# Performance work log

Measured on AMD Instinct MI355X. Metric: run time of the kernel, lower is better.

Reference implementation:

```python
import jax, jax.numpy as jnp
import numpy as np

WS = 16; HEADS = 6; TOPK = 64; KIN = 128; EPS = 1e-10
B, C, H, W = 1, 192, 192, 192
HID = 4 * C  # mlp_ratio * dim


def _ln(x, g, b):
    m = jnp.mean(x, axis=-1, keepdims=True)
    v = jnp.var(x, axis=-1, keepdims=True)
    return (x - m) * jax.lax.rsqrt(v + 1e-5) * g + b


def _dw_gelu(x, hw, w, b):
    # depthwise 5x5 conv + exact GELU on token sequence (B, N, C)
    Bx, N, Cx = x.shape
    h, wd = hw
    xi = x.transpose(0, 2, 1).reshape(Bx, Cx, h, wd)
    y = jax.lax.conv_general_dilated(xi, w, (1, 1), 'SAME',
        feature_group_count=Cx, dimension_numbers=('NCHW', 'OIHW', 'NCHW'))
    y = jax.nn.gelu(y + b[None, :, None, None], approximate=False)
    return y.reshape(Bx, Cx, N).transpose(0, 2, 1)


def _window_partition(x):
    b, h, w, c = x.shape
    x = x.reshape(b, h // WS, WS, w // WS, WS, c)
    return x.transpose(0, 1, 3, 2, 4, 5).reshape(-1, WS * WS, c)


def _window_reverse(win, h, w):
    c = win.shape[-1]
    b = win.shape[0] // ((h // WS) * (w // WS))
    x = win.reshape(b, h // WS, w // WS, WS, WS, c)
    return x.transpose(0, 1, 3, 2, 4, 5).reshape(b, h, w, c)


def setup_inputs():
    key = jax.random.key(0)
    ks = jax.random.split(key, 16)
    b_, n = B * (H // WS) * (W // WS), WS * WS
    wgen = lambda k, sh: jax.random.normal(k, sh, jnp.float32) * 0.02
    p = {}
    p['features_mv'] = jax.random.normal(ks[0], (B, C, H, W), jnp.float32)
    p['pfa_values'] = jax.random.uniform(ks[1], (b_, HEADS, n, KIN), jnp.float32)
    p['pfa_indices'] = jax.random.randint(ks[2], (b_, HEADS, n, KIN), 0, n, jnp.int32)
    p['rpi'] = jax.random.randint(ks[3], (n, n), 0, (2 * WS - 1) ** 2, jnp.int32)
    p['ln1_g'] = jnp.ones((C,)); p['ln1_b'] = jnp.zeros((C,))
    p['Wq_w'] = wgen(ks[4], (C, C)); p['Wq_b'] = jnp.zeros((C,))
    p['Wk_w'] = wgen(ks[5], (C, C)); p['Wk_b'] = jnp.zeros((C,))
    p['Wv_w'] = wgen(ks[6], (C, C)); p['Wv_b'] = jnp.zeros((C,))
    p['lepe_w'] = wgen(ks[7], (C, 1, 5, 5)); p['lepe_b'] = jnp.zeros((C,))
    p['rpb_table'] = wgen(ks[8], ((2 * WS - 1) ** 2, HEADS))
    p['proj_w'] = wgen(ks[9], (C, C)); p['proj_b'] = jnp.zeros((C,))
    p['ln2_g'] = jnp.ones((C,)); p['ln2_b'] = jnp.zeros((C,))
    p['fc1_w'] = wgen(ks[10], (C, HID)); p['fc1_b'] = jnp.zeros((HID,))
    p['ffn_dw_w'] = wgen(ks[11], (HID, 1, 5, 5)); p['ffn_dw_b'] = jnp.zeros((HID,))
    p['fc2_w'] = wgen(ks[12], (HID, C)); p['fc2_b'] = jnp.zeros((C,))
    return p


def reference(features_mv, pfa_values, pfa_indices, rpi, ln1_g, ln1_b,
              Wq_w, Wq_b, Wk_w, Wk_b, Wv_w, Wv_b, lepe_w, lepe_b, rpb_table,
              proj_w, proj_b, ln2_g, ln2_b, fc1_w, fc1_b, ffn_dw_w, ffn_dw_b,
              fc2_w, fc2_b):
    b, c, h, w = features_mv.shape
    hd = c // HEADS
    x = features_mv.reshape(b, c, h * w).transpose(0, 2, 1)  # (B, HW, C)
    shortcut = x
    xn = _ln(x, ln1_g, ln1_b)
    q = xn @ Wq_w + Wq_b
    k = xn @ Wk_w + Wk_b
    v = xn @ Wv_w + Wv_b
    vl = _dw_gelu(v, (h, w), lepe_w, lepe_b)  # v_LePE
    qkvp = jnp.concatenate([q, k, v, vl], axis=-1).reshape(b, h, w, 4 * c)
    xw = _window_partition(qkvp)  # (b_, n, 4C)
    b_, n = xw.shape[0], WS * WS
    qkvp = xw.reshape(b_, n, 4, HEADS, hd).transpose(2, 0, 3, 1, 4)
    q, k, v, vl = qkvp[0] * hd ** -0.5, qkvp[1], qkvp[2], qkvp[3]
    # SMM_QmK: per-query gathered q.k — dense scores then index gather
    scores = jnp.einsum('bhid,bhjd->bhij', q, k)          # (b_, H, n, n)
    attn = jnp.take_along_axis(scores, pfa_indices, axis=-1)  # (b_, H, n, K)
    # relative position bias, gathered by the same sparse indices
    rpb = rpb_table[rpi.reshape(-1)].reshape(n, n, HEADS).transpose(2, 0, 1)
    rpb_g = jnp.take_along_axis(jnp.broadcast_to(rpb[None], (b_, HEADS, n, n)),
                                pfa_indices, axis=-1)
    attn = jax.nn.softmax(attn + rpb_g, axis=-1)
    # progressive focused attention: multiply by prior values, renormalize
    attn = attn * pfa_values
    attn = (attn + EPS) / (jnp.sum(attn, axis=-1, keepdims=True) + EPS)
    # in-layer top-k reselection (topk=64 < KIN=128)
    tv, ti = jax.lax.top_k(attn, TOPK)
    idx = jnp.take_along_axis(pfa_indices, ti, axis=-1)   # (b_, H, n, TOPK)
    # SMM_AmV: scatter sparse attn to dense (duplicates sum) then matmul
    BH = b_ * HEADS
    a = tv.reshape(BH, n, TOPK)
    idxf = idx.reshape(BH, n, TOPK)
    dense = jnp.zeros((BH, n, n), tv.dtype).at[
        jnp.arange(BH)[:, None, None], jnp.arange(n)[None, :, None], idxf].add(a)
    xo = jnp.einsum('bij,bjd->bid', dense, v.reshape(BH, n, hd))
    xo = xo.reshape(b_, HEADS, n, hd) + vl
    xo = xo.transpose(0, 2, 1, 3).reshape(b_, n, c) @ proj_w + proj_b
    xr = _window_reverse(xo.reshape(-1, WS, WS, c), h, w)
    x = shortcut + xr.reshape(b, h * w, c)
    # ConvFFN
    y = _ln(x, ln2_g, ln2_b) @ fc1_w + fc1_b
    y = jax.nn.gelu(y, approximate=False)
    y = y + _dw_gelu(y, (h, w), ffn_dw_w, ffn_dw_b)
    x = x + (y @ fc2_w + fc2_b)
    return x
```

## Files before the change

kernel.cpp:

```cpp
#include <hip/hip_runtime.h>
#include <math.h>

#define HW 36864
#define CD 192
#define NH 6
#define HDIM 32
#define HIDD 768

typedef unsigned short u16;
typedef __attribute__((ext_vector_type(8))) short bf16x8;
typedef __attribute__((ext_vector_type(4))) float f32x4;

__device__ __forceinline__ float gelu_f(float x) {
  return 0.5f * x * (1.0f + erff(x * 0.70710678118654752f));
}
__device__ __forceinline__ u16 f2b(float f) {
  union { float f; unsigned u; } v; v.f = f;
  unsigned r = v.u + 0x7fff + ((v.u >> 16) & 1);
  return (u16)(r >> 16);
}
__device__ __forceinline__ float b2f(u16 b) {
  union { unsigned u; float f; } v; v.u = ((unsigned)b) << 16;
  return v.f;
}
__device__ __forceinline__ unsigned pack_hi16(unsigned w_lo, unsigned w_hi) {
  return __builtin_amdgcn_perm(w_hi, w_lo, 0x07060302u);
}

__global__ __launch_bounds__(256)
void lnt_kernel(const float* __restrict__ in, const float* __restrict__ g,
                const float* __restrict__ b, u16* __restrict__ outTM)
{
  __shared__ float tile[64][193];
  __shared__ float red[64][8];
  __shared__ float2 stat2[64];
  __shared__ float gb[384];
  const int tid = threadIdx.x;
  const int part = tid >> 6, tk = tid & 63;
  const int tok = blockIdx.x * 64 + tk;
  if (tid < 192) { gb[tid] = g[tid]; gb[192 + tid] = b[tid]; }
  float s = 0.f, sq = 0.f;
  for (int c = part * 48; c < part * 48 + 48; ++c) {
    float v = in[(size_t)c * HW + tok];
    tile[tk][c] = v; s += v; sq += v * v;
  }
  red[tk][part] = s; red[tk][4 + part] = sq;
  __syncthreads();
  if (tid < 64) {
    float ss = red[tid][0] + red[tid][1] + red[tid][2] + red[tid][3];
    float qq = red[tid][4] + red[tid][5] + red[tid][6] + red[tid][7];
    float m = ss * (1.0f / CD);
    float var = fmaxf(qq * (1.0f / CD) - m * m, 0.f);
    stat2[tid] = make_float2(m, rsqrtf(var + 1e-5f));
  }
  __syncthreads();
  unsigned* op = (unsigned*)outTM + (size_t)blockIdx.x * 6144;
  #pragma unroll
  for (int r = 0; r < 24; ++r) {
    int idx = tid + r * 256;
    int tok2 = idx / 96, dc = idx - tok2 * 96;
    float2 st = stat2[tok2];
    int c = dc * 2;
    float v0 = (tile[tok2][c] - st.x) * st.y * gb[c] + gb[192 + c];
    float v1 = (tile[tok2][c + 1] - st.x) * st.y * gb[c + 1] + gb[192 + c + 1];
    op[idx] = (unsigned)f2b(v0) | ((unsigned)f2b(v1) << 16);
  }
}

__global__ __launch_bounds__(256)
void trans_kernel(const u16* __restrict__ in, u16* __restrict__ out, int C)
{
  __shared__ u16 ls[64][34];
  const int m0 = blockIdx.x * 64, c0 = blockIdx.y * 32;
  const int t = threadIdx.x;
  #pragma unroll
  for (int r = 0; r < 4; ++r) {
    int idx = t + r * 256;
    int c = idx >> 5, dm = idx & 31;
    unsigned d = *(const unsigned*)(in + (size_t)(c0 + c) * HW + m0 + dm * 2);
    ls[dm * 2][c] = (u16)d;
    ls[dm * 2 + 1][c] = (u16)(d >> 16);
  }
  __syncthreads();
  #pragma unroll
  for (int r = 0; r < 4; ++r) {
    int idx = t + r * 256;
    int m = idx >> 4, dc = idx & 15;
    unsigned d = (unsigned)ls[m][dc * 2] | ((unsigned)ls[m][dc * 2 + 1] << 16);
    *(unsigned*)(out + (size_t)(m0 + m) * C + c0 + dc * 2) = d;
  }
}

__global__ __launch_bounds__(256)
void wtrans_kernel(const float* __restrict__ in, u16* __restrict__ out, int K, int N)
{
  __shared__ float ls[32][33];
  const int k0 = blockIdx.x * 32, n0 = blockIdx.y * 32;
  const int t = threadIdx.x;
  #pragma unroll
  for (int r = 0; r < 4; ++r) {
    int idx = t + r * 256;
    int k = idx >> 5, n = idx & 31;
    ls[k][n] = in[(size_t)(k0 + k) * N + n0 + n];
  }
  __syncthreads();
  #pragma unroll
  for (int r = 0; r < 4; ++r) {
    int idx = t + r * 256;
    int n = idx >> 5, k = idx & 31;
    out[(size_t)(n0 + n) * K + k0 + k] = f2b(ls[k][n]);
  }
}

__global__ __launch_bounds__(256)
void wtrans4_kernel(const float* __restrict__ w0, const float* __restrict__ w1,
                    const float* __restrict__ w2, const float* __restrict__ w3,
                    u16* __restrict__ out)
{
  __shared__ float ls[32][33];
  const int z = blockIdx.z;
  const float* in = (z == 0) ? w0 : (z == 1 ? w1 : (z == 2 ? w2 : w3));
  u16* op = out + (size_t)z * CD * CD;
  const int k0 = blockIdx.x * 32, n0 = blockIdx.y * 32;
  const int t = threadIdx.x;
  #pragma unroll
  for (int r = 0; r < 4; ++r) {
    int idx = t + r * 256;
    int k = idx >> 5, n = idx & 31;
    ls[k][n] = in[(size_t)(k0 + k) * CD + n0 + n];
  }
  __syncthreads();
  #pragma unroll
  for (int r = 0; r < 4; ++r) {
    int idx = t + r * 256;
    int n = idx >> 5, k = idx & 31;
    op[(size_t)(n0 + n) * CD + k0 + k] = f2b(ls[k][n]);
  }
}

template<int MODE>
__global__ __launch_bounds__(256, 4)
void mgemm_kernel(const u16* __restrict__ A,
                  const u16* __restrict__ W0, const u16* __restrict__ W1, const u16* __restrict__ W2,
                  const float* __restrict__ b0, const float* __restrict__ b1, const float* __restrict__ b2,
                  const float* __restrict__ aux, void* __restrict__ outv,
                  int K, int segN)
{
  const int n0 = blockIdx.x * 64;
  const int m0 = blockIdx.y * 128;
  const int seg = n0 / segN;
  const u16* Wp = (seg == 0) ? W0 : (seg == 1 ? W1 : W2);
  const float* biasp = (seg == 0) ? b0 : (seg == 1 ? b1 : b2);
  const int nl0 = n0 - seg * segN;

  __shared__ u16 As[128 * 32];
  __shared__ u16 Bs[64 * 32];

  const int tid = threadIdx.x;
  const int lane = tid & 63, wave = tid >> 6;
  const int wm = (wave >> 1) * 64, wn = (wave & 1) * 32;
  const int fm = lane & 15, fq = lane >> 4;
  const int ar = tid >> 2, akq = tid & 3;

  f32x4 acc[4][2];
  #pragma unroll
  for (int i = 0; i < 4; ++i) { acc[i][0] = (f32x4)(0.f); acc[i][1] = (f32x4)(0.f); }

  uint4 rA0, rA1, rB, nA0, nA1, nB;
  rA0 = *(const uint4*)(A + (size_t)(m0 + ar) * K + akq * 8);
  rA1 = *(const uint4*)(A + (size_t)(m0 + ar + 64) * K + akq * 8);
  rB  = *(const uint4*)(Wp + (size_t)(nl0 + ar) * K + akq * 8);

  for (int k0 = 0; k0 < K; k0 += 32) {
    *(uint4*)(&As[ar * 32 + akq * 8]) = rA0;
    *(uint4*)(&As[(ar + 64) * 32 + akq * 8]) = rA1;
    *(uint4*)(&Bs[ar * 32 + akq * 8]) = rB;
    __syncthreads();
    const int kn = (k0 + 32 < K) ? k0 + 32 : k0;
    nA0 = *(const uint4*)(A + (size_t)(m0 + ar) * K + kn + akq * 8);
    nA1 = *(const uint4*)(A + (size_t)(m0 + ar + 64) * K + kn + akq * 8);
    nB  = *(const uint4*)(Wp + (size_t)(nl0 + ar) * K + kn + akq * 8);
    bf16x8 af[4], bf[2];
    #pragma unroll
    for (int mt = 0; mt < 4; ++mt)
      af[mt] = *(const bf16x8*)(&As[(wm + mt * 16 + fm) * 32 + fq * 8]);
    #pragma unroll
    for (int nt = 0; nt < 2; ++nt)
      bf[nt] = *(const bf16x8*)(&Bs[(wn + nt * 16 + fm) * 32 + fq * 8]);
    #pragma unroll
    for (int mt = 0; mt < 4; ++mt)
      #pragma unroll
      for (int nt = 0; nt < 2; ++nt)
        acc[mt][nt] = __builtin_amdgcn_mfma_f32_16x16x32_bf16(af[mt], bf[nt], acc[mt][nt], 0, 0, 0);
    __syncthreads();
    rA0 = nA0; rA1 = nA1; rB = nB;
  }

  #pragma unroll
  for (int nt = 0; nt < 2; ++nt) {
    const int n = n0 + wn + nt * 16 + fm;
    const float bia = biasp[nl0 + wn + nt * 16 + fm];
    #pragma unroll
    for (int mt = 0; mt < 4; ++mt) {
      const int mb = m0 + wm + mt * 16 + fq * 4;
      float o[4];
      #pragma unroll
      for (int r = 0; r < 4; ++r) o[r] = acc[mt][nt][r] + bia;
      if (MODE == 0) {
        const float sc = (seg == 0) ? 0.17677669529663689f : 1.0f;
        u16 h0 = f2b(o[0] * sc), h1 = f2b(o[1] * sc), h2 = f2b(o[2] * sc), h3 = f2b(o[3] * sc);
        uint2 pk = make_uint2((unsigned)h0 | ((unsigned)h1 << 16), (unsigned)h2 | ((unsigned)h3 << 16));
        *(uint2*)((u16*)outv + (size_t)n * HW + mb) = pk;
      } else if (MODE == 1) {
        const float4 ax = *(const float4*)(aux + (size_t)n * HW + mb);
        *(float4*)((float*)outv + (size_t)n * HW + mb) =
            make_float4(o[0] + ax.x, o[1] + ax.y, o[2] + ax.z, o[3] + ax.w);
      } else if (MODE == 2) {
        u16 h0 = f2b(gelu_f(o[0])), h1 = f2b(gelu_f(o[1]));
        u16 h2 = f2b(gelu_f(o[2])), h3 = f2b(gelu_f(o[3]));
        uint2 pk = make_uint2((unsigned)h0 | ((unsigned)h1 << 16), (unsigned)h2 | ((unsigned)h3 << 16));
        *(uint2*)((u16*)outv + (size_t)n * HW + mb) = pk;
      } else {
        const float4 ax = *(const float4*)(aux + (size_t)n * HW + mb);
        float* op = (float*)outv;
        op[(size_t)(mb + 0) * CD + n] = o[0] + ax.x;
        op[(size_t)(mb + 1) * CD + n] = o[1] + ax.y;
        op[(size_t)(mb + 2) * CD + n] = o[2] + ax.z;
        op[(size_t)(mb + 3) * CD + n] = o[3] + ax.w;
      }
    }
  }
}

template<bool ADD>
__global__ __launch_bounds__(256)
void dwconv_kernel(const u16* __restrict__ in, const float* __restrict__ w,
                   const float* __restrict__ bias, u16* __restrict__ out)
{
  const int plane = blockIdx.z;
  const int bx = blockIdx.x * 64, by = blockIdx.y * 4;
  __shared__ float tile[8][68];
  __shared__ float ws[26];
  const int tid = threadIdx.x;
  if (tid < 26) ws[tid] = (tid < 25) ? w[plane * 25 + tid] : bias[plane];
  const u16* ip = in + (size_t)plane * HW;
  for (int e = tid; e < 544; e += 256) {
    int r = e / 68, cc = e - r * 68;
    int gy = by + r - 2, gx = bx + cc - 2;
    tile[r][cc] = (gy >= 0 && gy < 192 && gx >= 0 && gx < 192) ? b2f(ip[gy * 192 + gx]) : 0.f;
  }
  __syncthreads();
  const int tx = tid & 63, ty = tid >> 6;
  float acc = 0.f;
  #pragma unroll
  for (int dy = 0; dy < 5; ++dy)
    #pragma unroll
    for (int dx = 0; dx < 5; ++dx)
      acc = fmaf(tile[ty + dy][tx + dx], ws[dy * 5 + dx], acc);
  float v = gelu_f(acc + ws[25]);
  if (ADD) v += tile[ty + 2][tx + 2];
  out[(size_t)plane * HW + (by + ty) * 192 + bx + tx] = f2b(v);
}

__global__ __launch_bounds__(512, 6)
void attn_kernel(const u16* __restrict__ qg, const u16* __restrict__ kg,
                 const u16* __restrict__ vg, const u16* __restrict__ vlg,
                 const float* __restrict__ pfa_v, const int* __restrict__ pfa_i,
                 const int* __restrict__ rpi, const float* __restrict__ rpb_t,
                 u16* __restrict__ attn_out)
{
  const int h = blockIdx.x;
  const int win = blockIdx.y;
  const int wy = (win / 12) * 16;
  const int wx = (win - (win / 12) * 12) * 16;
  const size_t hb = (size_t)h * HDIM * HW;

  __shared__ u16 vT[32][264];
  __shared__ float Sb[32][262];
  __shared__ float rpb_h[964];

  const int tid = threadIdx.x;
  const int lane = tid & 63, wave = tid >> 6;
  const int fm = lane & 15, fq = lane >> 4;

  for (int r = tid; r < 961; r += 512) rpb_h[r] = rpb_t[r * 6 + h];

  u16* kst = (u16*)&Sb[0][0];
  #pragma unroll
  for (int r = 0; r < 8; ++r) {
    int idx = tid + r * 512;
    int d = idx >> 7, jp = idx & 127, j = jp * 2;
    int pg = (wy + (j >> 4)) * 192 + (wx + (j & 15));
    ushort2 kv = *(const ushort2*)(kg + hb + (size_t)d * HW + pg);
    kst[j * 32 + d] = kv.x; kst[(j + 1) * 32 + d] = kv.y;
    *(ushort2*)&vT[d][j] = *(const ushort2*)(vg + hb + (size_t)d * HW + pg);
  }
  __syncthreads();

  bf16x8 kf[4];
  #pragma unroll
  for (int t = 0; t < 4; ++t) {
    const int j0 = ((wave >> 1) * 4 + t) * 16;
    kf[t] = *(const bf16x8*)&kst[(j0 + fm) * 32 + fq * 8];
  }

  const size_t wb = ((size_t)win * NH + h) * 256;
  const unsigned long long lmlt = (1ull << lane) - 1ull;

  for (int pass = 0; pass < 8; ++pass) {
    union { bf16x8 v; u16 hh[8]; } aqu;
    {
      const int pgq = (wy + pass * 2 + (wave & 1)) * 192 + wx + fm;
      #pragma unroll
      for (int e = 0; e < 8; ++e)
        aqu.hh[e] = qg[hb + (size_t)(fq * 8 + e) * HW + pgq];
    }
    __syncthreads();

    int pj1[4], pj2[4]; float pv1[4], pv2[4];
    #pragma unroll
    for (int u = 0; u < 4; ++u) {
      const int i = pass * 32 + u * 8 + wave;
      const size_t base = (wb + (size_t)i) * 128;
      pj1[u] = pfa_i[base + lane];  pj2[u] = pfa_i[base + 64 + lane];
      pv1[u] = pfa_v[base + lane];  pv2[u] = pfa_v[base + 64 + lane];
    }

    #pragma unroll
    for (int t = 0; t < 4; ++t) {
      f32x4 c = __builtin_amdgcn_mfma_f32_16x16x32_bf16(aqu.v, kf[t], (f32x4)(0.f), 0, 0, 0);
      const int col = ((wave >> 1) * 4 + t) * 16 + fm;
      const int rowb = (wave & 1) * 16 + fq * 4;
      Sb[rowb + 0][col] = c[0]; Sb[rowb + 1][col] = c[1];
      Sb[rowb + 2][col] = c[2]; Sb[rowb + 3][col] = c[3];
    }
    __syncthreads();

    float rb1[4], rb2[4];
    #pragma unroll
    for (int u = 0; u < 4; ++u) {
      const int i = pass * 32 + u * 8 + wave;
      rb1[u] = rpb_h[rpi[i * 256 + pj1[u]]];
      rb2[u] = rpb_h[rpi[i * 256 + pj2[u]]];
    }
    float s1[4], s2[4];
    #pragma unroll
    for (int u = 0; u < 4; ++u) {
      const int iq = u * 8 + wave;
      s1[u] = Sb[iq][pj1[u]] + rb1[u];
      s2[u] = Sb[iq][pj2[u]] + rb2[u];
    }
    {
      const float2 z2 = make_float2(0.f, 0.f);
      #pragma unroll
      for (int u = 0; u < 4; ++u) {
        const int iq = u * 8 + wave;
        *(float2*)&Sb[iq][lane * 4]     = z2;
        *(float2*)&Sb[iq][lane * 4 + 2] = z2;
      }
    }
    float mx[4];
    #pragma unroll
    for (int u = 0; u < 4; ++u) mx[u] = fmaxf(s1[u], s2[u]);
    #pragma unroll
    for (int o = 32; o > 0; o >>= 1)
      #pragma unroll
      for (int u = 0; u < 4; ++u) mx[u] = fmaxf(mx[u], __shfl_xor(mx[u], o));
    float e1[4], e2[4], sA[4], sB[4];
    #pragma unroll
    for (int u = 0; u < 4; ++u) {
      e1[u] = expf(s1[u] - mx[u]); e2[u] = expf(s2[u] - mx[u]);
      sA[u] = e1[u] + e2[u];
      sB[u] = e1[u] * pv1[u] + e2[u] * pv2[u];
    }
    #pragma unroll
    for (int o = 32; o > 0; o >>= 1)
      #pragma unroll
      for (int u = 0; u < 4; ++u) { sA[u] += __shfl_xor(sA[u], o); sB[u] += __shfl_xor(sB[u], o); }
    unsigned ub1[4], ub2[4]; float a1[4], a2[4];
    #pragma unroll
    for (int u = 0; u < 4; ++u) {
      const float rs = 1.0f / sA[u];
      const float rden = 1.0f / (sB[u] * rs + 1e-10f);
      a1[u] = (e1[u] * rs * pv1[u] + 1e-10f) * rden;
      a2[u] = (e2[u] * rs * pv2[u] + 1e-10f) * rden;
      ub1[u] = __float_as_uint(a1[u]); ub2[u] = __float_as_uint(a2[u]);
    }
    unsigned thr[4] = {0u, 0u, 0u, 0u};
    #pragma unroll 1
    for (int bit = 30; bit >= 0; --bit) {
      #pragma unroll
      for (int u = 0; u < 4; ++u) {
        const unsigned cand = thr[u] | (1u << bit);
        const int cnt = (int)__popcll(__ballot(ub1[u] >= cand)) +
                        (int)__popcll(__ballot(ub2[u] >= cand));
        thr[u] = (cnt >= 64) ? cand : thr[u];
      }
    }
    #pragma unroll
    for (int u = 0; u < 4; ++u) {
      const int iq = u * 8 + wave;
      const bool gt1 = ub1[u] > thr[u], gt2 = ub2[u] > thr[u];
      const bool eq1 = ub1[u] == thr[u], eq2 = ub2[u] == thr[u];
      const unsigned long long meq1 = __ballot(eq1), meq2 = __ballot(eq2);
      const int need = 64 - (int)__popcll(__ballot(gt1)) - (int)__popcll(__ballot(gt2));
      const bool sel1 = gt1 || (eq1 && (int)__popcll(meq1 & lmlt) < need);
      const bool sel2 = gt2 || (eq2 && ((int)__popcll(meq1) + (int)__popcll(meq2 & lmlt)) < need);
      if (sel1) atomicAdd(&Sb[iq][pj1[u]], a1[u]);
      if (sel2) atomicAdd(&Sb[iq][pj2[u]], a2[u]);
    }
    __syncthreads();

    if (wave < 4) {
      const int mt = wave & 1, nt = wave >> 1;
      f32x4 acc = (f32x4)(0.f);
      #pragma unroll
      for (int k0 = 0; k0 < 8; ++k0) {
        const bf16x8 av = *(const bf16x8*)&vT[mt * 16 + fm][k0 * 32 + fq * 8];
        const float* pr = &Sb[nt * 16 + fm][k0 * 32 + fq * 8];
        const float2 p01 = *(const float2*)(pr + 0);
        const float2 p23 = *(const float2*)(pr + 2);
        const float2 p45 = *(const float2*)(pr + 4);
        const float2 p67 = *(const float2*)(pr + 6);
        const unsigned u0 = __float_as_uint(p01.x), u1 = __float_as_uint(p01.y);
        const unsigned u2 = __float_as_uint(p23.x), u3 = __float_as_uint(p23.y);
        const unsigned u4 = __float_as_uint(p45.x), u5 = __float_as_uint(p45.y);
        const unsigned u6 = __float_as_uint(p67.x), u7 = __float_as_uint(p67.y);
        union { bf16x8 v; unsigned q[4]; } bh, bl;
        bh.q[0] = pack_hi16(u0, u1); bh.q[1] = pack_hi16(u2, u3);
        bh.q[2] = pack_hi16(u4, u5); bh.q[3] = pack_hi16(u6, u7);
        const float l0 = p01.x - __uint_as_float(u0 & 0xffff0000u);
        const float l1 = p01.y - __uint_as_float(u1 & 0xffff0000u);
        const float l2 = p23.x - __uint_as_float(u2 & 0xffff0000u);
        const float l3 = p23.y - __uint_as_float(u3 & 0xffff0000u);
        const float l4 = p45.x - __uint_as_float(u4 & 0xffff0000u);
        const float l5 = p45.y - __uint_as_float(u5 & 0xffff0000u);
        const float l6 = p67.x - __uint_as_float(u6 & 0xffff0000u);
        const float l7 = p67.y - __uint_as_float(u7 & 0xffff0000u);
        bl.q[0] = pack_hi16(__float_as_uint(l0), __float_as_uint(l1));
        bl.q[1] = pack_hi16(__float_as_uint(l2), __float_as_uint(l3));
        bl.q[2] = pack_hi16(__float_as_uint(l4), __float_as_uint(l5));
        bl.q[3] = pack_hi16(__float_as_uint(l6), __float_as_uint(l7));
        acc = __builtin_amdgcn_mfma_f32_16x16x32_bf16(av, bh.v, acc, 0, 0, 0);
        acc = __builtin_amdgcn_mfma_f32_16x16x32_bf16(av, bl.v, acc, 0, 0, 0);
      }
      const int pg = (wy + pass * 2 + nt) * 192 + wx + fm;
      const int d0 = mt * 16 + fq * 4;
      const float r0 = acc[0] + b2f(vlg[hb + (size_t)(d0 + 0) * HW + pg]);
      const float r1 = acc[1] + b2f(vlg[hb + (size_t)(d0 + 1) * HW + pg]);
      const float r2 = acc[2] + b2f(vlg[hb + (size_t)(d0 + 2) * HW + pg]);
      const float r3 = acc[3] + b2f(vlg[hb + (size_t)(d0 + 3) * HW + pg]);
      const unsigned o01 = (unsigned)f2b(r0) | ((unsigned)f2b(r1) << 16);
      const unsigned o23 = (unsigned)f2b(r2) | ((unsigned)f2b(r3) << 16);
      *(uint2*)(attn_out + (size_t)pg * CD + h * HDIM + d0) = make_uint2(o01, o23);
    }
  }
}

extern "C" void kernel_launch(void* const* d_in, const int* in_sizes, int n_in,
                              void* d_out, int out_size, void* d_ws, size_t ws_size,
                              hipStream_t stream)
{
  (void)in_sizes; (void)n_in; (void)out_size; (void)ws_size;
  const float* features = (const float*)d_in[0];
  const float* pfa_v    = (const float*)d_in[1];
  const int*   pfa_i    = (const int*)d_in[2];
  const int*   rpi      = (const int*)d_in[3];
  const float* ln1_g    = (const float*)d_in[4];
  const float* ln1_b    = (const float*)d_in[5];
  const float* Wq_w     = (const float*)d_in[6];
  const float* Wq_b     = (const float*)d_in[7];
  const float* Wk_w     = (const float*)d_in[8];
  const float* Wk_b     = (const float*)d_in[9];
  const float* Wv_w     = (const float*)d_in[10];
  const float* Wv_b     = (const float*)d_in[11];
  const float* lepe_w   = (const float*)d_in[12];
  const float* lepe_b   = (const float*)d_in[13];
  const float* rpb_t    = (const float*)d_in[14];
  const float* proj_w   = (const float*)d_in[15];
  const float* proj_b   = (const float*)d_in[16];
  const float* ln2_g    = (const float*)d_in[17];
  const float* ln2_b    = (const float*)d_in[18];
  const float* fc1_w    = (const float*)d_in[19];
  const float* fc1_b    = (const float*)d_in[20];
  const float* dw_w     = (const float*)d_in[21];
  const float* dw_b     = (const float*)d_in[22];
  const float* fc2_w    = (const float*)d_in[23];
  const float* fc2_b    = (const float*)d_in[24];

  char* ws = (char*)d_ws;
  const size_t S  = (size_t)HW * CD;
  const size_t SB = S * 4;
  u16*   xnt    = (u16*)(ws);
  u16*   qkvb   = (u16*)(ws + SB / 2);
  u16*   q_ = qkvb; u16* k_ = qkvb + S; u16* v_ = qkvb + 2 * S;
  u16*   vl     = (u16*)(ws + 2 * SB);
  u16*   attn_o = (u16*)(ws + 2 * SB + SB / 2);
  float* x2     = (float*)(ws + 3 * SB);
  u16*   xn2t   = (u16*)(ws + 4 * SB);
  u16*   y_     = (u16*)(ws + 4 * SB + SB / 2);
  u16*   y2_    = (u16*)(ws + 6 * SB + SB / 2);
  u16*   y2t    = (u16*)(ws);
  u16*   wqt  = (u16*)(ws + 8 * SB + SB / 2);
  u16*   wkt  = wqt + 36864;
  u16*   wvt  = wkt + 36864;
  u16*   wpt  = wvt + 36864;
  u16*   wf1t = wpt + 36864;
  u16*   wf2t = wf1t + 147456;
  float* out = (float*)d_out;

  wtrans4_kernel<<<dim3(6, 6, 4), 256, 0, stream>>>(Wq_w, Wk_w, Wv_w, proj_w, wqt);
  wtrans_kernel<<<dim3(6, 24), 256, 0, stream>>>(fc1_w, wf1t, 192, 768);
  wtrans_kernel<<<dim3(24, 6), 256, 0, stream>>>(fc2_w, wf2t, 768, 192);
  lnt_kernel<<<dim3(HW / 64), 256, 0, stream>>>(features, ln1_g, ln1_b, xnt);
  mgemm_kernel<0><<<dim3(9, HW / 128), 256, 0, stream>>>(xnt, wqt, wkt, wvt, Wq_b, Wk_b, Wv_b,
                                                         nullptr, qkvb, 192, 192);
  dwconv_kernel<false><<<dim3(3, 48, 192), 256, 0, stream>>>(v_, lepe_w, lepe_b, vl);
  attn_kernel<<<dim3(6, 144), 512, 0, stream>>>(q_, k_, v_, vl, pfa_v, pfa_i, rpi, rpb_t, attn_o);
  mgemm_kernel<1><<<dim3(3, HW / 128), 256, 0, stream>>>(attn_o, wpt, wpt, wpt, proj_b, proj_b, proj_b,
                                                         features, x2, 192, 1 << 30);
  lnt_kernel<<<dim3(HW / 64), 256, 0, stream>>>(x2, ln2_g, ln2_b, xn2t);
  mgemm_kernel<2><<<dim3(12, HW / 128), 256, 0, stream>>>(xn2t, wf1t, wf1t, wf1t, fc1_b, fc1_b, fc1_b,
                                                          nullptr, y_, 192, 1 << 30);
  dwconv_kernel<true><<<dim3(3, 48, 768), 256, 0, stream>>>(y_, dw_w, dw_b, y2_);
  trans_kernel<<<dim3(HW / 64, 24), 256, 0, stream>>>(y2_, y2t, HIDD);
  mgemm_kernel<3><<<dim3(3, HW / 128), 256, 0, stream>>>(y2t, wf2t, wf2t, wf2t, fc2_b, fc2_b, fc2_b,
                                                         x2, out, 768, 1 << 30);
}
```

Baseline: 835.3 us.

## Prefetch attention inputs, shorten top-k radix search, use single fp16 MFMA for AV

```diff
diff --git a/kernel.cpp b/kernel.cpp
--- a/kernel.cpp
+++ b/kernel.cpp
@@ -10,6 +10,8 @@
 typedef unsigned short u16;
 typedef __attribute__((ext_vector_type(8))) short bf16x8;
 typedef __attribute__((ext_vector_type(4))) float f32x4;
+typedef __attribute__((ext_vector_type(8))) _Float16 f16x8;
+typedef __attribute__((ext_vector_type(2))) __fp16 fp16x2;
 
 __device__ __forceinline__ float gelu_f(float x) {
   return 0.5f * x * (1.0f + erff(x * 0.70710678118654752f));
@@ -23,8 +25,10 @@
   union { unsigned u; float f; } v; v.u = ((unsigned)b) << 16;
   return v.f;
 }
-__device__ __forceinline__ unsigned pack_hi16(unsigned w_lo, unsigned w_hi) {
-  return __builtin_amdgcn_perm(w_hi, w_lo, 0x07060302u);
+__device__ __forceinline__ unsigned pkrtz_u(float a, float b) {
+  union { fp16x2 h; unsigned u; } cv;
+  cv.h = __builtin_amdgcn_cvt_pkrtz(a, b);
+  return cv.u;
 }
 
 __global__ __launch_bounds__(256)
@@ -275,15 +279,15 @@
   const int wx = (win - (win / 12) * 12) * 16;
   const size_t hb = (size_t)h * HDIM * HW;
 
+  __shared__ float Sb[32][262];
   __shared__ u16 vT[32][264];
-  __shared__ float Sb[32][262];
-  __shared__ float rpb_h[964];
+  __shared__ u16 rpb_h[962];
 
   const int tid = threadIdx.x;
   const int lane = tid & 63, wave = tid >> 6;
   const int fm = lane & 15, fq = lane >> 4;
 
-  for (int r = tid; r < 961; r += 512) rpb_h[r] = rpb_t[r * 6 + h];
+  for (int r = tid; r < 961; r += 512) rpb_h[r] = f2b(rpb_t[r * 6 + h]);
 
   u16* kst = (u16*)&Sb[0][0];
   #pragma unroll
@@ -292,8 +296,9 @@
     int d = idx >> 7, jp = idx & 127, j = jp * 2;
     int pg = (wy + (j >> 4)) * 192 + (wx + (j & 15));
     ushort2 kv = *(const ushort2*)(kg + hb + (size_t)d * HW + pg);
-    kst[j * 32 + d] = kv.x; kst[(j + 1) * 32 + d] = kv.y;
-    *(ushort2*)&vT[d][j] = *(const ushort2*)(vg + hb + (size_t)d * HW + pg);
+    kst[j * 40 + d] = kv.x; kst[(j + 1) * 40 + d] = kv.y;
+    ushort2 vv = *(const ushort2*)(vg + hb + (size_t)d * HW + pg);
+    *(unsigned*)&vT[d][j] = pkrtz_u(b2f(vv.x), b2f(vv.y));
   }
   __syncthreads();
 
@@ -301,11 +306,20 @@
   #pragma unroll
   for (int t = 0; t < 4; ++t) {
     const int j0 = ((wave >> 1) * 4 + t) * 16;
-    kf[t] = *(const bf16x8*)&kst[(j0 + fm) * 32 + fq * 8];
+    kf[t] = *(const bf16x8*)&kst[(j0 + fm) * 40 + fq * 8];
   }
 
   const size_t wb = ((size_t)win * NH + h) * 256;
   const unsigned long long lmlt = (1ull << lane) - 1ull;
+  const unsigned KMASK = 0xFFFFF800u;
+
+  int pj1[4], pj2[4]; float pv1[4], pv2[4];
+  #pragma unroll
+  for (int u = 0; u < 4; ++u) {
+    const size_t base = (wb + (size_t)(u * 8 + wave)) * 128;
+    pj1[u] = pfa_i[base + lane];  pj2[u] = pfa_i[base + 64 + lane];
+    pv1[u] = pfa_v[base + lane];  pv2[u] = pfa_v[base + 64 + lane];
+  }
 
   for (int pass = 0; pass < 8; ++pass) {
     union { bf16x8 v; u16 hh[8]; } aqu;
@@ -315,15 +329,23 @@
       for (int e = 0; e < 8; ++e)
         aqu.hh[e] = qg[hb + (size_t)(fq * 8 + e) * HW + pgq];
     }
+    float vlv[4];
+    if (wave < 4) {
+      const int mt = wave & 1, nt = wave >> 1;
+      const int pgo = (wy + pass * 2 + nt) * 192 + wx + fm;
+      const int d0 = mt * 16 + fq * 4;
+      #pragma unroll
+      for (int e = 0; e < 4; ++e)
+        vlv[e] = b2f(vlg[hb + (size_t)(d0 + e) * HW + pgo]);
+    }
     __syncthreads();
 
-    int pj1[4], pj2[4]; float pv1[4], pv2[4];
+    int rbi1[4], rbi2[4];
     #pragma unroll
     for (int u = 0; u < 4; ++u) {
       const int i = pass * 32 + u * 8 + wave;
-      const size_t base = (wb + (size_t)i) * 128;
-      pj1[u] = pfa_i[base + lane];  pj2[u] = pfa_i[base + 64 + lane];
-      pv1[u] = pfa_v[base + lane];  pv2[u] = pfa_v[base + 64 + lane];
+      rbi1[u] = rpi[i * 256 + pj1[u]];
+      rbi2[u] = rpi[i * 256 + pj2[u]];
     }
 
     #pragma unroll
@@ -336,19 +358,12 @@
     }
     __syncthreads();
 
-    float rb1[4], rb2[4];
-    #pragma unroll
-    for (int u = 0; u < 4; ++u) {
-      const int i = pass * 32 + u * 8 + wave;
-      rb1[u] = rpb_h[rpi[i * 256 + pj1[u]]];
-      rb2[u] = rpb_h[rpi[i * 256 + pj2[u]]];
-    }
     float s1[4], s2[4];
     #pragma unroll
     for (int u = 0; u < 4; ++u) {
       const int iq = u * 8 + wave;
-      s1[u] = Sb[iq][pj1[u]] + rb1[u];
-      s2[u] = Sb[iq][pj2[u]] + rb2[u];
+      s1[u] = Sb[iq][pj1[u]] + b2f(rpb_h[rbi1[u]]);
+      s2[u] = Sb[iq][pj2[u]] + b2f(rpb_h[rbi2[u]]);
     }
     {
       const float2 z2 = make_float2(0.f, 0.f);
@@ -388,7 +403,7 @@
     }
     unsigned thr[4] = {0u, 0u, 0u, 0u};
     #pragma unroll 1
-    for (int bit = 30; bit >= 0; --bit) {
+    for (int bit = 29; bit >= 11; --bit) {
       #pragma unroll
       for (int u = 0; u < 4; ++u) {
         const unsigned cand = thr[u] | (1u << bit);
@@ -400,8 +415,9 @@
     #pragma unroll
     for (int u = 0; u < 4; ++u) {
       const int iq = u * 8 + wave;
-      const bool gt1 = ub1[u] > thr[u], gt2 = ub2[u] > thr[u];
-      const bool eq1 = ub1[u] == thr[u], eq2 = ub2[u] == thr[u];
+      const unsigned kb1 = ub1[u] & KMASK, kb2 = ub2[u] & KMASK;
+      const bool gt1 = kb1 > thr[u], gt2 = kb2 > thr[u];
+      const bool eq1 = kb1 == thr[u], eq2 = kb2 == thr[u];
       const unsigned long long meq1 = __ballot(eq1), meq2 = __ballot(eq2);
       const int need = 64 - (int)__popcll(__ballot(gt1)) - (int)__popcll(__ballot(gt2));
       const bool sel1 = gt1 || (eq1 && (int)__popcll(meq1 & lmlt) < need);
@@ -409,6 +425,16 @@
       if (sel1) atomicAdd(&Sb[iq][pj1[u]], a1[u]);
       if (sel2) atomicAdd(&Sb[iq][pj2[u]], a2[u]);
     }
+    int npj1[4], npj2[4]; float npv1[4], npv2[4];
+    {
+      const int pnext = (pass + 1) & 7;
+      #pragma unroll
+      for (int u = 0; u < 4; ++u) {
+        const size_t base = (wb + (size_t)(pnext * 32 + u * 8 + wave)) * 128;
+        npj1[u] = pfa_i[base + lane];  npj2[u] = pfa_i[base + 64 + lane];
+        npv1[u] = pfa_v[base + lane];  npv2[u] = pfa_v[base + 64 + lane];
+      }
+    }
     __syncthreads();
 
     if (wave < 4) {
@@ -416,43 +442,33 @@
       f32x4 acc = (f32x4)(0.f);
       #pragma unroll
       for (int k0 = 0; k0 < 8; ++k0) {
-        const bf16x8 av = *(const bf16x8*)&vT[mt * 16 + fm][k0 * 32 + fq * 8];
+        const f16x8 av = *(const f16x8*)&vT[mt * 16 + fm][k0 * 32 + fq * 8];
         const float* pr = &Sb[nt * 16 + fm][k0 * 32 + fq * 8];
         const float2 p01 = *(const float2*)(pr + 0);
         const float2 p23 = *(const float2*)(pr + 2);
         const float2 p45 = *(const float2*)(pr + 4);
         const float2 p67 = *(const float2*)(pr + 6);
-        const unsigned u0 = __float_as_uint(p01.x), u1 = __float_as_uint(p01.y);
-        const unsigned u2 = __float_as_uint(p23.x), u3 = __float_as_uint(p23.y);
-        const unsigned u4 = __float_as_uint(p45.x), u5 = __float_as_uint(p45.y);
-        const unsigned u6 = __float_as_uint(p67.x), u7 = __float_as_uint(p67.y);
-        union { bf16x8 v; unsigned q[4]; } bh, bl;
-        bh.q[0] = pack_hi16(u0, u1); bh.q[1] = pack_hi16(u2, u3);
-        bh.q[2] = pack_hi16(u4, u5); bh.q[3] = pack_hi16(u6, u7);
-        const float l0 = p01.x - __uint_as_float(u0 & 0xffff0000u);
-        const float l1 = p01.y - __uint_as_float(u1 & 0xffff0000u);
-        const float l2 = p23.x - __uint_as_float(u2 & 0xffff0000u);
-        const float l3 = p23.y - __uint_as_float(u3 & 0xffff0000u);
-        const float l4 = p45.x - __uint_as_float(u4 & 0xffff0000u);
-        const float l5 = p45.y - __uint_as_float(u5 & 0xffff0000u);
-        const float l6 = p67.x - __uint_as_float(u6 & 0xffff0000u);
-        const float l7 = p67.y - __uint_as_float(u7 & 0xffff0000u);
-        bl.q[0] = pack_hi16(__float_as_uint(l0), __float_as_uint(l1));
-        bl.q[1] = pack_hi16(__float_as_uint(l2), __float_as_uint(l3));
-        bl.q[2] = pack_hi16(__float_as_uint(l4), __float_as_uint(l5));
-        bl.q[3] = pack_hi16(__float_as_uint(l6), __float_as_uint(l7));
-        acc = __builtin_amdgcn_mfma_f32_16x16x32_bf16(av, bh.v, acc, 0, 0, 0);
-        acc = __builtin_amdgcn_mfma_f32_16x16x32_bf16(av, bl.v, acc, 0, 0, 0);
+        union { f16x8 v; unsigned q[4]; } bp;
+        bp.q[0] = pkrtz_u(p01.x, p01.y);
+        bp.q[1] = pkrtz_u(p23.x, p23.y);
+        bp.q[2] = pkrtz_u(p45.x, p45.y);
+        bp.q[3] = pkrtz_u(p67.x, p67.y);
+        acc = __builtin_amdgcn_mfma_f32_16x16x32_f16(av, bp.v, acc, 0, 0, 0);
       }
-      const int pg = (wy + pass * 2 + nt) * 192 + wx + fm;
+      const int pgo = (wy + pass * 2 + nt) * 192 + wx + fm;
       const int d0 = mt * 16 + fq * 4;
-      const float r0 = acc[0] + b2f(vlg[hb + (size_t)(d0 + 0) * HW + pg]);
-      const float r1 = acc[1] + b2f(vlg[hb + (size_t)(d0 + 1) * HW + pg]);
-      const float r2 = acc[2] + b2f(vlg[hb + (size_t)(d0 + 2) * HW + pg]);
-      const float r3 = acc[3] + b2f(vlg[hb + (size_t)(d0 + 3) * HW + pg]);
+      const float r0 = acc[0] + vlv[0];
+      const float r1 = acc[1] + vlv[1];
+      const float r2 = acc[2] + vlv[2];
+      const float r3 = acc[3] + vlv[3];
       const unsigned o01 = (unsigned)f2b(r0) | ((unsigned)f2b(r1) << 16);
       const unsigned o23 = (unsigned)f2b(r2) | ((unsigned)f2b(r3) << 16);
-      *(uint2*)(attn_out + (size_t)pg * CD + h * HDIM + d0) = make_uint2(o01, o23);
+      *(uint2*)(attn_out + (size_t)pgo * CD + h * HDIM + d0) = make_uint2(o01, o23);
+    }
+    #pragma unroll
+    for (int u = 0; u < 4; ++u) {
+      pj1[u] = npj1[u]; pj2[u] = npj2[u];
+      pv1[u] = npv1[u]; pv2[u] = npv2[u];
     }
   }
 }
```

New measurement: 801.4 us. -4.1%, faster.
